# Performance work log

Hardware: AMD Instinct MI355X
Metric: run time of the kernel (lower is better)

## Reference

```python
import jax, jax.numpy as jnp
import numpy as np

B, S, D, H = 4, 2048, 768, 8
HD = D // H
EPS = 1e-5
NEG = -1e9


def setup_inputs() -> dict:
    key = jax.random.key(0)
    ks = jax.random.split(key, 12)
    s = 1.0 / np.sqrt(D)
    inp = {
        "hidden_states": jax.random.normal(ks[0], (B, S, D), dtype=jnp.float32),
        "anchor_mask": jax.random.bernoulli(ks[1], 0.5, (B, S)),
        "ln_g": jnp.ones((D,), jnp.float32),
        "ln_b": jnp.zeros((D,), jnp.float32),
        "Wq": jax.random.uniform(ks[2], (D, D), jnp.float32, -s, s),
        "bq": jax.random.uniform(ks[3], (D,), jnp.float32, -s, s),
        "Wk": jax.random.uniform(ks[4], (D, D), jnp.float32, -s, s),
        "bk": jax.random.uniform(ks[5], (D,), jnp.float32, -s, s),
        "Wv": jax.random.uniform(ks[6], (D, D), jnp.float32, -s, s),
        "bv": jax.random.uniform(ks[7], (D,), jnp.float32, -s, s),
        "Wo": jax.random.uniform(ks[8], (D, D), jnp.float32, -s, s),
        "bo": jax.random.uniform(ks[9], (D,), jnp.float32, -s, s),
    }
    return inp


def reference(hidden_states, anchor_mask, ln_g, ln_b, Wq, bq, Wk, bk, Wv, bv, Wo, bo):
    # LayerNorm (per-token, so applying to all tokens == applying to gathered anchors)
    mu = jnp.mean(hidden_states, axis=-1, keepdims=True)
    var = jnp.mean(jnp.square(hidden_states - mu), axis=-1, keepdims=True)
    x = (hidden_states - mu) * jax.lax.rsqrt(var + EPS) * ln_g + ln_b

    # QKV projections: torch Linear is x @ W.T + b
    q = (jnp.einsum('bsd,ed->bse', x, Wq) + bq).reshape(B, S, H, HD)
    k = (jnp.einsum('bsd,ed->bse', x, Wk) + bk).reshape(B, S, H, HD)
    v = (jnp.einsum('bsd,ed->bse', x, Wv) + bv).reshape(B, S, H, HD)

    scale = 1.0 / np.sqrt(HD)
    scores = jnp.einsum('bqhd,bkhd->bhqk', q, k) * scale
    # keys restricted to anchor positions (equivalent to the gather)
    key_mask = anchor_mask[:, None, None, :]  # (B,1,1,S)
    scores = jnp.where(key_mask, scores, NEG)
    attn = jax.nn.softmax(scores, axis=-1)  # dropout is identity in eval

    out = jnp.einsum('bhqk,bkhd->bqhd', attn, v).reshape(B, S, D)
    out = jnp.einsum('bsd,ed->bse', out, Wo) + bo
    # scatter back: zeros at non-anchor positions
    return out * anchor_mask[:, :, None].astype(out.dtype)
```

## Files before the change

### kernel.cpp

```cpp
#include <hip/hip_runtime.h>
#include <math.h>

#define S_LEN 2048
#define D_DIM 768
#define NH 8
#define HD 96
#define NTOK 8192

typedef short bf16x8 __attribute__((ext_vector_type(8)));
typedef float f32x4 __attribute__((ext_vector_type(4)));
typedef float f32x16 __attribute__((ext_vector_type(16)));
typedef unsigned int u32x2 __attribute__((ext_vector_type(2)));
typedef unsigned int u32x4 __attribute__((ext_vector_type(4)));

__device__ __forceinline__ f32x4 mfma16(bf16x8 a, bf16x8 b, f32x4 c) {
    return __builtin_amdgcn_mfma_f32_16x16x32_bf16(a, b, c, 0, 0, 0);
}
__device__ __forceinline__ f32x16 mfma32(bf16x8 a, bf16x8 b, f32x16 c) {
    return __builtin_amdgcn_mfma_f32_32x32x16_bf16(a, b, c, 0, 0, 0);
}

__device__ __forceinline__ unsigned short f2bf(float f) {
    unsigned int u = __float_as_uint(f);
    u += 0x7fffu + ((u >> 16) & 1u);
    return (unsigned short)(u >> 16);
}

__device__ __forceinline__ unsigned int cvtpk(float lo, float hi) {
    unsigned int r;
    asm("v_cvt_pk_bf16_f32 %0, %1, %2" : "=v"(r) : "v"(lo), "v"(hi));
    return r;
}

__device__ __forceinline__ void gl_lds16(const unsigned short* g, unsigned short* l) {
    __builtin_amdgcn_global_load_lds(
        (const __attribute__((address_space(1))) unsigned int*)g,
        (__attribute__((address_space(3))) unsigned int*)l, 16, 0, 0);
}

#define TILE_SHORTS 6144
#define BH_SHORTS   196608

__global__ __launch_bounds__(256) void prep_kernel(
    const unsigned char* __restrict__ mb, int* __restrict__ idx, int* __restrict__ cnt,
    const float* __restrict__ Wq, const float* __restrict__ Wk,
    const float* __restrict__ Wv, const float* __restrict__ Wo,
    unsigned short* __restrict__ W4b, float* __restrict__ out)
{
    const int bi = blockIdx.x;
    const int t  = threadIdx.x;

    if (bi < 4) {
        __shared__ int red[4];
        __shared__ int warp_tot[4];
        const int b = bi;
        int s = 0;
        for (int i = t; i < NTOK; i += 256) s += (int)mb[i];
        for (int off = 32; off > 0; off >>= 1) s += __shfl_down(s, off, 64);
        if ((t & 63) == 0) red[t >> 6] = s;
        __syncthreads();
        const int total = red[0] + red[1] + red[2] + red[3];
        const int mode = (total > 20000) ? 2 : ((total > 2500) ? 1 : 0);
        const int*   mi = (const int*)mb;
        const float* mf = (const float*)mb;
        const int p0 = t * 8;
        int av = 0, c = 0;
        #pragma unroll
        for (int j = 0; j < 8; ++j) {
            const int g = b * S_LEN + p0 + j;
            bool a;
            if (mode == 2)      a = (mf[g] != 0.0f);
            else if (mode == 1) a = (mb[g] != 0);
            else                a = (mi[g] != 0);
            if (a) { av |= (1 << j); ++c; }
        }
        const int lane = t & 63, w = t >> 6;
        int v = c;
        #pragma unroll
        for (int off = 1; off < 64; off <<= 1) {
            const int u = __shfl_up(v, off, 64);
            if (lane >= off) v += u;
        }
        if (lane == 63) warp_tot[w] = v;
        __syncthreads();
        int wbase = 0;
        for (int i = 0; i < w; ++i) wbase += warp_tot[i];
        int o = wbase + v - c;
        #pragma unroll
        for (int j = 0; j < 8; ++j)
            if (av & (1 << j)) idx[b * S_LEN + (o++)] = p0 + j;
        if (t == 255) cnt[b] = wbase + v;
    } else if (bi < 1156) {
        const int i = bi - 4;
        const int w = i / 288, blk = i % 288;
        const float* src = (w == 0) ? Wq : (w == 1) ? Wk : (w == 2) ? Wv : Wo;
        const int base = (blk * 256 + t) * 8;
        const float4 a = *(const float4*)&src[base];
        const float4 c = *(const float4*)&src[base + 4];
        uint4 u;
        u.x = (unsigned int)f2bf(a.x) | ((unsigned int)f2bf(a.y) << 16);
        u.y = (unsigned int)f2bf(a.z) | ((unsigned int)f2bf(a.w) << 16);
        u.z = (unsigned int)f2bf(c.x) | ((unsigned int)f2bf(c.y) << 16);
        u.w = (unsigned int)f2bf(c.z) | ((unsigned int)f2bf(c.w) << 16);
        *(uint4*)&W4b[(size_t)w * 589824 + base] = u;
    } else {
        const size_t i4 = (size_t)(bi - 1156) * 256 + t;
        float4 z; z.x = z.y = z.z = z.w = 0.0f;
        *(float4*)&out[i4 * 4] = z;
    }
}

__global__ __launch_bounds__(256) void ln_gather_kernel(
    const float* __restrict__ H, const float* __restrict__ g,
    const float* __restrict__ bta, const int* __restrict__ idx,
    const int* __restrict__ cnt, unsigned short* __restrict__ X)
{
    __shared__ float rs[4], rss[4];
    const int slot = blockIdx.x;
    const int b = slot >> 11, r = slot & (S_LEN - 1);
    if (r >= cnt[b]) return;
    const int p = idx[slot];
    const float* hr = H + (size_t)(b * S_LEN + p) * D_DIM;
    unsigned short* xr = X + (size_t)slot * D_DIM;
    const int t = threadIdx.x;
    const float v0 = hr[t], v1 = hr[t + 256], v2 = hr[t + 512];
    float s  = v0 + v1 + v2;
    float ss = v0*v0 + v1*v1 + v2*v2;
    for (int off = 32; off > 0; off >>= 1) {
        s  += __shfl_down(s,  off, 64);
        ss += __shfl_down(ss, off, 64);
    }
    if ((t & 63) == 0) { rs[t >> 6] = s; rss[t >> 6] = ss; }
    __syncthreads();
    const float sum = rs[0] + rs[1] + rs[2] + rs[3];
    const float sq  = rss[0] + rss[1] + rss[2] + rss[3];
    const float mu  = sum * (1.0f / D_DIM);
    const float var = sq * (1.0f / D_DIM) - mu * mu;
    const float rstd = rsqrtf(var + 1e-5f);
    xr[t]       = f2bf((v0 - mu) * rstd * g[t]       + bta[t]);
    xr[t + 256] = f2bf((v1 - mu) * rstd * g[t + 256] + bta[t + 256]);
    xr[t + 512] = f2bf((v2 - mu) * rstd * g[t + 512] + bta[t + 512]);
}

__global__ __launch_bounds__(256) void gemm_bf16(
    const unsigned short* __restrict__ A,
    const unsigned short* __restrict__ W4,
    const float* __restrict__ b0, const float* __restrict__ b1,
    const float* __restrict__ b2,
    const int* __restrict__ cnt, const int* __restrict__ idx,
    unsigned short* __restrict__ Qo, unsigned short* __restrict__ Kp,
    unsigned short* __restrict__ Vp, float* __restrict__ Fo,
    int oproj)
{
    const int z = blockIdx.z;
    const int m0 = blockIdx.y * 128;
    const int b  = m0 >> 11;
    const int rbase = m0 & (S_LEN - 1);
    const int nc = cnt[b];
    if (rbase >= nc) return;
    const int n0 = blockIdx.x * 128;
    const unsigned short* W = W4 + (size_t)z * 589824;
    const float* bias = (z == 0) ? b0 : (z == 1 ? b1 : b2);

    __shared__ unsigned short Al[128 * 32];
    __shared__ unsigned short Bl[128 * 32];

    const int t = threadIdx.x;
    const int srow = t >> 2, sg = t & 3;
    const int ra0 = b * S_LEN + min(rbase + srow,      nc - 1);
    const int ra1 = b * S_LEN + min(rbase + srow + 64, nc - 1);
    const unsigned short* gA0 = A + (size_t)ra0 * 768 + sg * 8;
    const unsigned short* gA1 = A + (size_t)ra1 * 768 + sg * 8;
    const unsigned short* gB0 = W + (size_t)(n0 + srow)      * 768 + sg * 8;
    const unsigned short* gB1 = W + (size_t)(n0 + srow + 64) * 768 + sg * 8;
    unsigned short* lA = Al + t * 8;
    unsigned short* lB = Bl + t * 8;

    const int w = t >> 6, lane = t & 63;
    const int l15 = lane & 15, quad = lane >> 4;
    const int mh = (w & 1) * 64, nh2 = (w >> 1) * 64;

    f32x4 acc[4][4] = {};

    int aoff[4], boff[4];
    #pragma unroll
    for (int i = 0; i < 4; ++i) {
        aoff[i] = (mh  + i * 16 + l15) * 32 + quad * 8;
        boff[i] = (nh2 + i * 16 + l15) * 32 + quad * 8;
    }

    for (int k0 = 0; k0 < 768; k0 += 32) {
        __syncthreads();
        gl_lds16(gA0 + k0, lA);
        gl_lds16(gA1 + k0, lA + 2048);
        gl_lds16(gB0 + k0, lB);
        gl_lds16(gB1 + k0, lB + 2048);
        __syncthreads();
        bf16x8 af[4], bfr[4];
        #pragma unroll
        for (int i = 0; i < 4; ++i) af[i]  = *(const bf16x8*)(Al + aoff[i]);
        #pragma unroll
        for (int i = 0; i < 4; ++i) bfr[i] = *(const bf16x8*)(Bl + boff[i]);
        #pragma unroll
        for (int ms = 0; ms < 4; ++ms)
            #pragma unroll
            for (int ns = 0; ns < 4; ++ns)
                acc[ms][ns] = mfma16(af[ms], bfr[ns], acc[ms][ns]);
    }

    if (!oproj) {
        if (z == 0) {
            #pragma unroll
            for (int ns = 0; ns < 4; ++ns) {
                const int n = n0 + nh2 + ns * 16 + l15;
                const float bv = bias[n];
                #pragma unroll
                for (int ms = 0; ms < 4; ++ms) {
                    const int ml = mh + ms * 16 + quad * 4;
                    #pragma unroll
                    for (int r = 0; r < 4; ++r) {
                        const int slot = b * S_LEN + rbase + ml + r;
                        Qo[(size_t)slot * 768 + n] = f2bf(acc[ms][ns][r] + bv);
                    }
                }
            }
        } else if (z == 1) {
            #pragma unroll
            for (int ns = 0; ns < 4; ++ns) {
                const int n = n0 + nh2 + ns * 16 + l15;
                const int h = n / 96, d = n - h * 96;
                const float bv = bias[n];
                unsigned short* base = Kp + (size_t)(b * 8 + h) * BH_SHORTS;
                const int dseg = d >> 3, dlo = d & 7;
                #pragma unroll
                for (int ms = 0; ms < 4; ++ms) {
                    const int ml = mh + ms * 16 + quad * 4;
                    #pragma unroll
                    for (int r = 0; r < 4; ++r) {
                        const int tok = rbase + ml + r;
                        const int kt = tok >> 6, tk = tok & 63;
                        const int g16 = tk >> 4, lr = tk & 15;
                        base[(size_t)kt * TILE_SHORTS +
                             (g16 * 192 + dseg * 16 + lr) * 8 + dlo] =
                            (tok < nc) ? f2bf(acc[ms][ns][r] + bv)
                                       : (unsigned short)0;
                    }
                }
            }
        } else {
            #pragma unroll
            for (int ns = 0; ns < 4; ++ns) {
                const int n = n0 + nh2 + ns * 16 + l15;
                const int h = n / 96, d = n - h * 96;
                const float bv = bias[n];
                unsigned short* base = Vp + (size_t)(b * 8 + h) * BH_SHORTS;
                const int dg = d >> 4, l16 = d & 15;
                #pragma unroll
                for (int ms = 0; ms < 4; ++ms) {
                    const int ml = mh + ms * 16 + quad * 4;
                    const int k = rbase + ml;
                    const int kt = k >> 6, tk = k & 63;
                    const int kseg = tk >> 3, klo = tk & 7;
                    const unsigned short h0 =
                        (k + 0 < nc) ? f2bf(acc[ms][ns][0] + bv) : (unsigned short)0;
                    const unsigned short h1 =
                        (k + 1 < nc) ? f2bf(acc[ms][ns][1] + bv) : (unsigned short)0;
                    const unsigned short h2 =
                        (k + 2 < nc) ? f2bf(acc[ms][ns][2] + bv) : (unsigned short)0;
                    const unsigned short h3 =
                        (k + 3 < nc) ? f2bf(acc[ms][ns][3] + bv) : (unsigned short)0;
                    uint2 u;
                    u.x = (unsigned int)h0 | ((unsigned int)h1 << 16);
                    u.y = (unsigned int)h2 | ((unsigned int)h3 << 16);
                    *(uint2*)&base[(size_t)kt * TILE_SHORTS +
                                   (dg * 128 + kseg * 16 + l16) * 8 + klo] = u;
                }
            }
        }
    } else {
        #pragma unroll
        for (int ns = 0; ns < 4; ++ns) {
            const int n = n0 + nh2 + ns * 16 + l15;
            const float bv = bias[n];
            #pragma unroll
            for (int ms = 0; ms < 4; ++ms) {
                const int ml = mh + ms * 16 + quad * 4;
                #pragma unroll
                for (int r = 0; r < 4; ++r) {
                    const int rloc = rbase + ml + r;
                    if (rloc < nc) {
                        const int orow = b * S_LEN + idx[b * S_LEN + rloc];
                        Fo[(size_t)orow * 768 + n] = acc[ms][ns][r] + bv;
                    }
                }
            }
        }
    }
}

__global__ __launch_bounds__(128) void attn_mfma(
    const unsigned short* __restrict__ Q,
    const unsigned short* __restrict__ Kp,
    const unsigned short* __restrict__ Vp,
    const int* __restrict__ cnt,
    unsigned short* __restrict__ O)
{
    const int bh = blockIdx.x & 31;
    const int b  = bh >> 3, h = bh & 7;
    const int q0 = (blockIdx.x >> 5) * 64;
    const int nk = cnt[b];
    if (q0 >= nk) return;

    __shared__ unsigned short SB[2 * 12288];

    const int t = threadIdx.x, w = t >> 6, lane = t & 63;
    const int l15 = lane & 15;
    const int gh  = (lane >> 4) & 1;
    const int hi  = lane >> 5;
    const int q32 = lane & 31;
    const int qw  = q0 + w * 32;
    const int bS  = b * S_LEN;
    const float CE = 0.14724459f;

    const int t8 = t * 8;
    const unsigned short* Kst = Kp + (size_t)(b * 8 + h) * BH_SHORTS + t8;
    const unsigned short* Vst = Vp + (size_t)(b * 8 + h) * BH_SHORTS + t8;

    const unsigned short* qrow = Q + (size_t)(bS + qw + q32) * 768 + h * 96 + hi * 8;
    bf16x8 qf[6];
    #pragma unroll
    for (int ks = 0; ks < 6; ++ks) qf[ks] = *(const bf16x8*)(qrow + ks * 16);

    const int kb0 = (gh * 192 + hi * 16 + l15) * 8;
    const int vb0 = (gh * 128 + hi * 16 + l15) * 8;

    unsigned short* bufA = SB;
    unsigned short* bufB = SB + 12288;

    float ls0 = 0.0f, ls1 = 0.0f;
    f32x16 oacc[3] = {};

    const int kts = (nk + 63) >> 6;

    #pragma unroll
    for (int r = 0; r < 6; ++r) {
        gl_lds16(Kst + r * 1024, bufA + r * 1024 + t8);
        gl_lds16(Vst + r * 1024, bufA + 6144 + r * 1024 + t8);
    }
    Kst += TILE_SHORTS; Vst += TILE_SHORTS;
    __syncthreads();

    for (int kt = 0; kt < kts; ++kt) {
        if (kt + 1 < kts) {
            #pragma unroll
            for (int r = 0; r < 6; ++r) {
                gl_lds16(Kst + r * 1024, bufB + r * 1024 + t8);
                gl_lds16(Vst + r * 1024, bufB + 6144 + r * 1024 + t8);
            }
            Kst += TILE_SHORTS; Vst += TILE_SHORTS;
        }
        const unsigned short* Kl = bufA;
        const unsigned short* Vl = bufA + 6144;

        #pragma unroll
        for (int s = 0; s < 2; ++s) {
            f32x16 sa = {};
            __builtin_amdgcn_s_setprio(1);
            #pragma unroll
            for (int ks = 0; ks < 6; ++ks) {
                const bf16x8 kf = *(const bf16x8*)(Kl + kb0 + (s * 384 + ks * 32) * 8);
                sa = mfma32(kf, qf[ks], sa);
            }
            __builtin_amdgcn_s_setprio(0);

            unsigned int wv[8];
            #pragma unroll
            for (int j = 0; j < 8; ++j) {
                const float e0 = exp2f(sa[2 * j]     * CE);
                const float e1 = exp2f(sa[2 * j + 1] * CE);
                if (j & 1) ls1 += e0 + e1; else ls0 += e0 + e1;
                wv[j] = cvtpk(e0, e1);
            }
            const u32x2 r02 = __builtin_amdgcn_permlane32_swap(wv[0], wv[2], false, false);
            const u32x2 r13 = __builtin_amdgcn_permlane32_swap(wv[1], wv[3], false, false);
            const u32x2 r46 = __builtin_amdgcn_permlane32_swap(wv[4], wv[6], false, false);
            const u32x2 r57 = __builtin_amdgcn_permlane32_swap(wv[5], wv[7], false, false);
            const u32x4 pw0 = { r02.x, r13.x, r02.y, r13.y };
            const u32x4 pw1 = { r46.x, r57.x, r46.y, r57.y };
            const bf16x8 pb0 = __builtin_bit_cast(bf16x8, pw0);
            const bf16x8 pb1 = __builtin_bit_cast(bf16x8, pw1);

            const int kkb = s * 2;
            __builtin_amdgcn_s_setprio(1);
            #pragma unroll
            for (int dg = 0; dg < 3; ++dg) {
                const bf16x8 v0 = *(const bf16x8*)(Vl + vb0 + (dg * 256 + kkb * 32) * 8);
                const bf16x8 v1 = *(const bf16x8*)(Vl + vb0 + (dg * 256 + (kkb + 1) * 32) * 8);
                oacc[dg] = mfma32(v0, pb0, oacc[dg]);
                oacc[dg] = mfma32(v1, pb1, oacc[dg]);
            }
            __builtin_amdgcn_s_setprio(0);
        }

        __syncthreads();
        unsigned short* tmp = bufA; bufA = bufB; bufB = tmp;
    }

    float lsum = ls0 + ls1;
    lsum += __shfl_xor(lsum, 32);
    lsum -= (float)((kts << 6) - nk);

    const int qi = qw + q32;
    if (qi < nk) {
        const float rl = 1.0f / lsum;
        unsigned short* og = O + (size_t)(bS + qi) * 768 + h * 96;
        #pragma unroll
        for (int dg = 0; dg < 3; ++dg) {
            #pragma unroll
            for (int m = 0; m < 4; ++m) {
                uint2 u;
                u.x = cvtpk(oacc[dg][4 * m]     * rl, oacc[dg][4 * m + 1] * rl);
                u.y = cvtpk(oacc[dg][4 * m + 2] * rl, oacc[dg][4 * m + 3] * rl);
                *(uint2*)&og[dg * 32 + m * 8 + hi * 4] = u;
            }
        }
    }
}

extern "C" void kernel_launch(void* const* d_in, const int* in_sizes, int n_in,
                              void* d_out, int out_size, void* d_ws, size_t ws_size,
                              hipStream_t stream)
{
    const float* hs  = (const float*)d_in[0];
    const unsigned char* am = (const unsigned char*)d_in[1];
    const float* lng = (const float*)d_in[2];
    const float* lnb = (const float*)d_in[3];
    const float* Wq  = (const float*)d_in[4];
    const float* bq  = (const float*)d_in[5];
    const float* Wk  = (const float*)d_in[6];
    const float* bk  = (const float*)d_in[7];
    const float* Wv  = (const float*)d_in[8];
    const float* bv  = (const float*)d_in[9];
    const float* Wo  = (const float*)d_in[10];
    const float* bo  = (const float*)d_in[11];

    char* ws = (char*)d_ws;
    const size_t BUF = (size_t)NTOK * 768 * 2;
    int* idx = (int*)ws;
    int* cnt = (int*)(ws + 32768);
    unsigned short* xb  = (unsigned short*)(ws + 65536);
    unsigned short* Qb  = (unsigned short*)(ws + 65536 + BUF);
    unsigned short* Kpb = (unsigned short*)(ws + 65536 + 2 * BUF);
    unsigned short* Vpb = (unsigned short*)(ws + 65536 + 3 * BUF);
    unsigned short* W4b = (unsigned short*)(ws + 65536 + 4 * BUF);
    unsigned short* Ob  = xb;
    float* out = (float*)d_out;

    prep_kernel<<<dim3(2692), dim3(256), 0, stream>>>(
        am, idx, cnt, Wq, Wk, Wv, Wo, W4b, out);

    ln_gather_kernel<<<dim3(NTOK), dim3(256), 0, stream>>>(hs, lng, lnb, idx, cnt, xb);

    gemm_bf16<<<dim3(6, 64, 3), dim3(256), 0, stream>>>(
        xb, W4b, bq, bk, bv, cnt, idx, Qb, Kpb, Vpb, nullptr, 0);

    attn_mfma<<<dim3(1024), dim3(128), 0, stream>>>(Qb, Kpb, Vpb, cnt, Ob);

    gemm_bf16<<<dim3(6, 64, 1), dim3(256), 0, stream>>>(
        Ob, W4b + (size_t)3 * 589824, bo, bo, bo, cnt, idx,
        nullptr, nullptr, nullptr, out, 1);
}
```

Before: 204.8 us.

## Split attention keys across four waves per 32-query block with LDS reduction

Each block now handles 32 queries with 256 threads. The four waves take interleaved key tiles and read K/V fragments straight from global memory instead of staging them through double-buffered LDS. Partial output accumulators and row sums are then combined with a two-step tree reduction through shared memory. The aim is more parallelism and occupancy on a short-sequence attention with no online max. The cost is uncoalesced direct global loads without LDS staging, plus extra reduction and synchronisation overhead.

```diff
diff --git a/kernel.cpp b/kernel.cpp
--- a/kernel.cpp
+++ b/kernel.cpp
@@ -298,7 +298,7 @@
     }
 }
 
-__global__ __launch_bounds__(128) void attn_mfma(
+__global__ __launch_bounds__(256) void attn_mfma(
     const unsigned short* __restrict__ Q,
     const unsigned short* __restrict__ Kp,
     const unsigned short* __restrict__ Vp,
@@ -307,26 +307,24 @@
 {
     const int bh = blockIdx.x & 31;
     const int b  = bh >> 3, h = bh & 7;
-    const int q0 = (blockIdx.x >> 5) * 64;
+    const int q0 = (blockIdx.x >> 5) * 32;
     const int nk = cnt[b];
     if (q0 >= nk) return;
 
-    __shared__ unsigned short SB[2 * 12288];
+    __shared__ f32x4 CMB4[2][64][13];
 
     const int t = threadIdx.x, w = t >> 6, lane = t & 63;
     const int l15 = lane & 15;
     const int gh  = (lane >> 4) & 1;
     const int hi  = lane >> 5;
     const int q32 = lane & 31;
-    const int qw  = q0 + w * 32;
     const int bS  = b * S_LEN;
     const float CE = 0.14724459f;
 
-    const int t8 = t * 8;
-    const unsigned short* Kst = Kp + (size_t)(b * 8 + h) * BH_SHORTS + t8;
-    const unsigned short* Vst = Vp + (size_t)(b * 8 + h) * BH_SHORTS + t8;
-
-    const unsigned short* qrow = Q + (size_t)(bS + qw + q32) * 768 + h * 96 + hi * 8;
+    const unsigned short* Kg = Kp + (size_t)(b * 8 + h) * BH_SHORTS;
+    const unsigned short* Vg = Vp + (size_t)(b * 8 + h) * BH_SHORTS;
+
+    const unsigned short* qrow = Q + (size_t)(bS + q0 + q32) * 768 + h * 96 + hi * 8;
     bf16x8 qf[6];
     #pragma unroll
     for (int ks = 0; ks < 6; ++ks) qf[ks] = *(const bf16x8*)(qrow + ks * 16);
@@ -334,43 +332,25 @@
     const int kb0 = (gh * 192 + hi * 16 + l15) * 8;
     const int vb0 = (gh * 128 + hi * 16 + l15) * 8;
 
-    unsigned short* bufA = SB;
-    unsigned short* bufB = SB + 12288;
-
     float ls0 = 0.0f, ls1 = 0.0f;
     f32x16 oacc[3] = {};
 
     const int kts = (nk + 63) >> 6;
 
-    #pragma unroll
-    for (int r = 0; r < 6; ++r) {
-        gl_lds16(Kst + r * 1024, bufA + r * 1024 + t8);
-        gl_lds16(Vst + r * 1024, bufA + 6144 + r * 1024 + t8);
-    }
-    Kst += TILE_SHORTS; Vst += TILE_SHORTS;
-    __syncthreads();
-
-    for (int kt = 0; kt < kts; ++kt) {
-        if (kt + 1 < kts) {
-            #pragma unroll
-            for (int r = 0; r < 6; ++r) {
-                gl_lds16(Kst + r * 1024, bufB + r * 1024 + t8);
-                gl_lds16(Vst + r * 1024, bufB + 6144 + r * 1024 + t8);
-            }
-            Kst += TILE_SHORTS; Vst += TILE_SHORTS;
-        }
-        const unsigned short* Kl = bufA;
-        const unsigned short* Vl = bufA + 6144;
+    for (int kt = w; kt < kts; kt += 4) {
+        const unsigned short* Kt = Kg + (size_t)kt * TILE_SHORTS + kb0;
+        const unsigned short* Vt = Vg + (size_t)kt * TILE_SHORTS + vb0;
 
         #pragma unroll
         for (int s = 0; s < 2; ++s) {
+            bf16x8 kf[6];
+            #pragma unroll
+            for (int ks = 0; ks < 6; ++ks)
+                kf[ks] = *(const bf16x8*)(Kt + (s * 384 + ks * 32) * 8);
             f32x16 sa = {};
             __builtin_amdgcn_s_setprio(1);
             #pragma unroll
-            for (int ks = 0; ks < 6; ++ks) {
-                const bf16x8 kf = *(const bf16x8*)(Kl + kb0 + (s * 384 + ks * 32) * 8);
-                sa = mfma32(kf, qf[ks], sa);
-            }
+            for (int ks = 0; ks < 6; ++ks) sa = mfma32(kf[ks], qf[ks], sa);
             __builtin_amdgcn_s_setprio(0);
 
             unsigned int wv[8];
@@ -394,23 +374,76 @@
             __builtin_amdgcn_s_setprio(1);
             #pragma unroll
             for (int dg = 0; dg < 3; ++dg) {
-                const bf16x8 v0 = *(const bf16x8*)(Vl + vb0 + (dg * 256 + kkb * 32) * 8);
-                const bf16x8 v1 = *(const bf16x8*)(Vl + vb0 + (dg * 256 + (kkb + 1) * 32) * 8);
+                const bf16x8 v0 = *(const bf16x8*)(Vt + (dg * 256 + kkb * 32) * 8);
+                const bf16x8 v1 = *(const bf16x8*)(Vt + (dg * 256 + (kkb + 1) * 32) * 8);
                 oacc[dg] = mfma32(v0, pb0, oacc[dg]);
                 oacc[dg] = mfma32(v1, pb1, oacc[dg]);
             }
             __builtin_amdgcn_s_setprio(0);
         }
-
-        __syncthreads();
-        unsigned short* tmp = bufA; bufA = bufB; bufB = tmp;
     }
 
     float lsum = ls0 + ls1;
     lsum += __shfl_xor(lsum, 32);
+
+    if (w >= 2) {
+        f32x4* dst = CMB4[w - 2][lane];
+        #pragma unroll
+        for (int dg = 0; dg < 3; ++dg)
+            #pragma unroll
+            for (int m = 0; m < 4; ++m) {
+                const f32x4 p = { oacc[dg][4 * m],     oacc[dg][4 * m + 1],
+                                  oacc[dg][4 * m + 2], oacc[dg][4 * m + 3] };
+                dst[dg * 4 + m] = p;
+            }
+        const f32x4 tl = { lsum, 0.0f, 0.0f, 0.0f };
+        dst[12] = tl;
+    }
+    __syncthreads();
+    if (w < 2) {
+        const f32x4* src = CMB4[w][lane];
+        #pragma unroll
+        for (int dg = 0; dg < 3; ++dg)
+            #pragma unroll
+            for (int m = 0; m < 4; ++m) {
+                const f32x4 p = src[dg * 4 + m];
+                #pragma unroll
+                for (int j = 0; j < 4; ++j) oacc[dg][4 * m + j] += p[j];
+            }
+        lsum += src[12][0];
+    }
+    __syncthreads();
+    if (w == 1) {
+        f32x4* dst = CMB4[0][lane];
+        #pragma unroll
+        for (int dg = 0; dg < 3; ++dg)
+            #pragma unroll
+            for (int m = 0; m < 4; ++m) {
+                const f32x4 p = { oacc[dg][4 * m],     oacc[dg][4 * m + 1],
+                                  oacc[dg][4 * m + 2], oacc[dg][4 * m + 3] };
+                dst[dg * 4 + m] = p;
+            }
+        const f32x4 tl = { lsum, 0.0f, 0.0f, 0.0f };
+        dst[12] = tl;
+    }
+    __syncthreads();
+    if (w > 0) return;
+
+    {
+        const f32x4* src = CMB4[0][lane];
+        #pragma unroll
+        for (int dg = 0; dg < 3; ++dg)
+            #pragma unroll
+            for (int m = 0; m < 4; ++m) {
+                const f32x4 p = src[dg * 4 + m];
+                #pragma unroll
+                for (int j = 0; j < 4; ++j) oacc[dg][4 * m + j] += p[j];
+            }
+        lsum += src[12][0];
+    }
     lsum -= (float)((kts << 6) - nk);
 
-    const int qi = qw + q32;
+    const int qi = q0 + q32;
     if (qi < nk) {
         const float rl = 1.0f / lsum;
         unsigned short* og = O + (size_t)(bS + qi) * 768 + h * 96;
@@ -464,7 +497,7 @@
     gemm_bf16<<<dim3(6, 64, 3), dim3(256), 0, stream>>>(
         xb, W4b, bq, bk, bv, cnt, idx, Qb, Kpb, Vpb, nullptr, 0);
 
-    attn_mfma<<<dim3(1024), dim3(128), 0, stream>>>(Qb, Kpb, Vpb, cnt, Ob);
+    attn_mfma<<<dim3(2048), dim3(256), 0, stream>>>(Qb, Kpb, Vpb, cnt, Ob);
 
     gemm_bf16<<<dim3(6, 64, 1), dim3(256), 0, stream>>>(
         Ob, W4b + (size_t)3 * 589824, bo, bo, bo, cnt, idx,
```

Result: faster. 196.2 us (-4.2%).
